# Kernel tuning notes

Hardware: AMD Instinct MI355X
Metric: run time of the kernel (lower is better)

The kernel has to match this reference:

```python
import jax, jax.numpy as jnp
import numpy as np

B, D, H, L = 65536, 512, 1024, 64
LOG2PI = float(np.log(2.0 * np.pi))


def setup_inputs() -> dict:
    key = jax.random.key(0)
    ks = jax.random.split(key, 16)
    s = jnp.float32(0.02)

    def w(k, shape):
        return jax.random.normal(k, shape, dtype=jnp.float32) * s

    return {
        "x": jax.random.normal(ks[0], (B, D), dtype=jnp.float32),
        "eps": jax.random.normal(ks[1], (B, L), dtype=jnp.float32),
        # encoder params (Linear stored as [in, out] for x @ W + b)
        "W_enc_h": w(ks[2], (D, H)), "b_enc_h": jnp.zeros((H,), jnp.float32),
        "W_enc_mu": w(ks[3], (H, L)), "b_enc_mu": jnp.zeros((L,), jnp.float32),
        "W_enc_lv": w(ks[4], (H, L)), "b_enc_lv": jnp.zeros((L,), jnp.float32),
        # decoder params
        "W_dec_h": w(ks[5], (L, H)), "b_dec_h": jnp.zeros((H,), jnp.float32),
        "W_dec_mu": w(ks[6], (H, D)), "b_dec_mu": jnp.zeros((D,), jnp.float32),
        "W_dec_lv": w(ks[7], (H, D)), "b_dec_lv": jnp.zeros((D,), jnp.float32),
    }


def reference(x, eps, W_enc_h, b_enc_h, W_enc_mu, b_enc_mu, W_enc_lv, b_enc_lv,
              W_dec_h, b_dec_h, W_dec_mu, b_dec_mu, W_dec_lv, b_dec_lv):
    beta = jnp.float32(1.0)
    # encoder
    h = jnp.tanh(x @ W_enc_h + b_enc_h)                      # [B, H]
    mu_z = h @ W_enc_mu + b_enc_mu                           # [B, L]
    lv_z = h @ W_enc_lv + b_enc_lv                           # [B, L]
    # reparameterised sample
    z = mu_z + jnp.exp(0.5 * lv_z) * eps                     # [B, L]
    # decoder
    hd = jnp.tanh(z @ W_dec_h + b_dec_h)                     # [B, H]
    mu_x = jax.nn.softmax(hd @ W_dec_mu + b_dec_mu, axis=-1) # [B, D]
    lv_x = hd @ W_dec_lv + b_dec_lv                          # [B, D]
    # KL(q(z|x) || N(0, I))
    kl = -0.5 * jnp.sum(1.0 + lv_z - mu_z ** 2 - jnp.exp(lv_z), axis=-1)  # [B]
    # diagonal Gaussian log-likelihood (closed form of MultivariateNormal
    # with diag_embed(exp(ln_var)) covariance)
    ln_pxz = -0.5 * jnp.sum(lv_x + (x - mu_x) ** 2 * jnp.exp(-lv_x) + LOG2PI, axis=-1)  # [B]
    return jnp.mean(ln_pxz - beta * kl)
```

## Files before the change

kernel.cpp:

```cpp
#include <hip/hip_runtime.h>

typedef unsigned char u8;
typedef unsigned short u16;
typedef unsigned int u32;
typedef long i64;
typedef __attribute__((ext_vector_type(2))) long long2v;
typedef __attribute__((ext_vector_type(4))) float floatx4;

#define LOG2PI_F 1.8378770664093453f

__device__ __forceinline__ u16 f2bf(float f) {
  union { float f; u32 i; } c; c.f = f;
  u32 i = c.i;
  u32 r = (i + 0x7fffu + ((i >> 16) & 1u)) >> 16;
  return (u16)r;
}
__device__ __forceinline__ float bf2f(u16 u) {
  union { u32 i; float f; } c; c.i = ((u32)u) << 16; return c.f;
}
__device__ __forceinline__ u8 f2fp8(float f) {
  int p = __builtin_amdgcn_cvt_pk_fp8_f32(f, f, 0, false);
  return (u8)(p & 0xff);
}
__device__ __forceinline__ u32 pk4fp8(float a, float b, float c, float d) {
  int lo = __builtin_amdgcn_cvt_pk_fp8_f32(a, b, 0, false);
  int v  = __builtin_amdgcn_cvt_pk_fp8_f32(c, d, lo, true);
  return (u32)v;
}
__device__ __forceinline__ void llds16(const void* g, void* l) {
  __builtin_amdgcn_global_load_lds(
      (const __attribute__((address_space(1))) u32*)g,
      (__attribute__((address_space(3))) u32*)l, 16, 0, 0);
}
__device__ __forceinline__ u32 permk(u32 k) {
  u32 g = k & ~63u, o = (k >> 3) & 7u, r = k & 7u;
  u32 po = ((o & 3u) << 1) | (o >> 2);
  return g | (po << 3) | r;
}

#define INV_4096  2.44140625e-4f
#define INV_16384 6.103515625e-5f

__global__ void pack_xb(const float* __restrict__ in, u32* __restrict__ out, int n4) {
  int i = blockIdx.x * 256 + threadIdx.x;
  if (i >= n4) return;
  const float4 v = ((const float4*)in)[i];
  int row = i >> 7;
  int k = (i & 127) << 2;
  int kp = permk(k);
  out[(row << 7) + (kp >> 2)] = pk4fp8(v.x * 16.f, v.y * 16.f, v.z * 16.f, v.w * 16.f);
}

__global__ void pack_wt(const float* __restrict__ W, u8* __restrict__ Wt, int K, int N) {
  int idx = blockIdx.x * 256 + threadIdx.x;
  if (idx >= K * N) return;
  int k = idx / N, n = idx - k * N;
  Wt[(size_t)n * K + permk(k)] = f2fp8(W[idx] * 256.f);
}

__global__ void pack_wt2(const float* __restrict__ W1, const float* __restrict__ W2,
                         u8* __restrict__ Wt, int K, int N1, int N2) {
  int idx = blockIdx.x * 256 + threadIdx.x;
  if (idx >= (N1 + N2) * K) return;
  int n = idx / K, k = idx - n * K;
  float v = (n < N1) ? W1[(size_t)k * N1 + n] : W2[(size_t)k * N2 + (n - N1)];
  Wt[(size_t)n * K + permk(k)] = f2fp8(v * 256.f);
}

__global__ void catf(const float* __restrict__ a, const float* __restrict__ b,
                     float* __restrict__ o, int n1, int n2) {
  int i = blockIdx.x * 256 + threadIdx.x;
  if (i < n1) o[i] = a[i];
  else if (i < n1 + n2) o[i] = b[i - n1];
}

template <int EPI>
__global__ __launch_bounds__(256) void gemm_bt(
    const u8* __restrict__ A, const u8* __restrict__ Bt,
    const float* __restrict__ bias, void* __restrict__ Cv,
    float inv, float outs, int M, int N, int K) {
  __shared__ __align__(16) u8 As[128 * 64];
  __shared__ __align__(16) u8 Bs[128 * 64];
  const int t = threadIdx.x;
  const int wave = t >> 6, lane = t & 63;
  const int quad = lane >> 4, l16 = lane & 15;
  const int bm = blockIdx.y * 128, bn = blockIdx.x * 128;
  const int wm = (wave >> 1) * 64, wn = (wave & 1) * 64;

  floatx4 acc[4][4];
#pragma unroll
  for (int i = 0; i < 4; ++i)
#pragma unroll
    for (int j = 0; j < 4; ++j) acc[i][j] = (floatx4){0.f, 0.f, 0.f, 0.f};

  for (int kt = 0; kt < K; kt += 64) {
#pragma unroll
    for (int i = 0; i < 2; ++i) {
      int c = i * 256 + t;
      int r = c >> 2, kcS = c & 3;
      int kc = kcS ^ ((r >> 1) & 3);
      llds16(A + (size_t)(bm + r) * K + kt + kc * 16, &As[c * 16]);
      llds16(Bt + (size_t)(bn + r) * K + kt + kc * 16, &Bs[c * 16]);
    }
    __builtin_amdgcn_s_waitcnt(0);
    __syncthreads();

    long2v a2[4], b2[4];
#pragma unroll
    for (int mi = 0; mi < 4; ++mi) {
      int m = wm + mi * 16 + l16;
      a2[mi] = *(const long2v*)&As[(4 * m + (quad ^ ((m >> 1) & 3))) * 16];
    }
#pragma unroll
    for (int ni = 0; ni < 4; ++ni) {
      int n = wn + ni * 16 + l16;
      b2[ni] = *(const long2v*)&Bs[(4 * n + (quad ^ ((n >> 1) & 3))) * 16];
    }
#pragma unroll
    for (int h = 0; h < 2; ++h)
#pragma unroll
      for (int mi = 0; mi < 4; ++mi)
#pragma unroll
        for (int ni = 0; ni < 4; ++ni)
          acc[mi][ni] = __builtin_amdgcn_mfma_f32_16x16x32_fp8_fp8(
              a2[mi][h], b2[ni][h], acc[mi][ni], 0, 0, 0);
    __syncthreads();
  }

#pragma unroll
  for (int ni = 0; ni < 4; ++ni) {
    int col = bn + wn + ni * 16 + l16;
    float bv = bias[col];
#pragma unroll
    for (int mi = 0; mi < 4; ++mi) {
#pragma unroll
      for (int r = 0; r < 4; ++r) {
        int row = bm + wm + mi * 16 + quad * 4 + r;
        float v = acc[mi][ni][r] * inv + bv;
        if (EPI == 0) {
          ((u8*)Cv)[(size_t)row * N + permk(col)] = f2fp8(tanhf(v) * outs);
        } else {
          ((u16*)Cv)[(size_t)row * N + col] = f2bf(v);
        }
      }
    }
  }
}

__global__ __launch_bounds__(256) void gemm_z(
    const u8* __restrict__ A, const u8* __restrict__ Bt,
    const float* __restrict__ bias, const float* __restrict__ eps,
    u8* __restrict__ z, float* __restrict__ accp, int M, int K) {
  __shared__ __align__(16) u8 As[128 * 64];
  __shared__ __align__(16) u8 Bs[128 * 64];
  __shared__ float sexp[128 * 64];
  const int t = threadIdx.x;
  const int wave = t >> 6, lane = t & 63;
  const int quad = lane >> 4, l16 = lane & 15;
  const int bm = blockIdx.y * 128;
  const int wm = (wave >> 1) * 64, wn = (wave & 1) * 64;

  floatx4 acc[4][4];
#pragma unroll
  for (int i = 0; i < 4; ++i)
#pragma unroll
    for (int j = 0; j < 4; ++j) acc[i][j] = (floatx4){0.f, 0.f, 0.f, 0.f};

  for (int kt = 0; kt < K; kt += 64) {
#pragma unroll
    for (int i = 0; i < 2; ++i) {
      int c = i * 256 + t;
      int r = c >> 2, kcS = c & 3;
      int kc = kcS ^ ((r >> 1) & 3);
      llds16(A + (size_t)(bm + r) * K + kt + kc * 16, &As[c * 16]);
      llds16(Bt + (size_t)r * K + kt + kc * 16, &Bs[c * 16]);
    }
    __builtin_amdgcn_s_waitcnt(0);
    __syncthreads();

    long2v a2[4], b2[4];
#pragma unroll
    for (int mi = 0; mi < 4; ++mi) {
      int m = wm + mi * 16 + l16;
      a2[mi] = *(const long2v*)&As[(4 * m + (quad ^ ((m >> 1) & 3))) * 16];
    }
#pragma unroll
    for (int ni = 0; ni < 4; ++ni) {
      int n = wn + ni * 16 + l16;
      b2[ni] = *(const long2v*)&Bs[(4 * n + (quad ^ ((n >> 1) & 3))) * 16];
    }
#pragma unroll
    for (int h = 0; h < 2; ++h)
#pragma unroll
      for (int mi = 0; mi < 4; ++mi)
#pragma unroll
        for (int ni = 0; ni < 4; ++ni)
          acc[mi][ni] = __builtin_amdgcn_mfma_f32_16x16x32_fp8_fp8(
              a2[mi][h], b2[ni][h], acc[mi][ni], 0, 0, 0);
    __syncthreads();
  }

  const bool is_lv = (wave & 1);
  float kl = 0.f;
#pragma unroll
  for (int ni = 0; ni < 4; ++ni) {
    int col = wn + ni * 16 + l16;
    float bv = bias[col];
#pragma unroll
    for (int mi = 0; mi < 4; ++mi) {
#pragma unroll
      for (int r = 0; r < 4; ++r) {
        int row = wm + mi * 16 + quad * 4 + r;
        float v = acc[mi][ni][r] * INV_16384 + bv;
        if (is_lv) {
          kl += 1.0f + v - __expf(v);
          sexp[row * 64 + (col - 64)] = __expf(0.5f * v);
        } else {
          kl -= v * v;
        }
      }
    }
  }
  __syncthreads();
  if (!is_lv) {
#pragma unroll
    for (int ni = 0; ni < 4; ++ni) {
      int col = wn + ni * 16 + l16;
      float bv = bias[col];
#pragma unroll
      for (int mi = 0; mi < 4; ++mi) {
#pragma unroll
        for (int r = 0; r < 4; ++r) {
          int row = wm + mi * 16 + quad * 4 + r;
          float mu = acc[mi][ni][r] * INV_16384 + bv;
          size_t grow = (size_t)(bm + row);
          float ep = eps[grow * 64 + col];
          z[grow * 64 + permk(col)] = f2fp8((mu + sexp[row * 64 + col] * ep) * 16.f);
        }
      }
    }
  }
  kl *= 0.5f;
  for (int off = 32; off > 0; off >>= 1) kl += __shfl_xor(kl, off, 64);
  __shared__ float s4[4];
  if (lane == 0) s4[wave] = kl;
  __syncthreads();
  if (t == 0) atomicAdd(accp, s4[0] + s4[1] + s4[2] + s4[3]);
}

__global__ __launch_bounds__(256) void lik_kernel(
    const u16* __restrict__ loglv, const float* __restrict__ x,
    float* __restrict__ acc) {
  typedef __attribute__((ext_vector_type(8))) short short8;
  const int wave = threadIdx.x >> 6, lane = threadIdx.x & 63;
  float wacc = 0.f;
  for (int rr = 0; rr < 8; ++rr) {
    int row = blockIdx.x * 32 + wave * 8 + rr;
    const u16* Lr = loglv + (size_t)row * 1024;
    short8 lg8 = ((const short8*)Lr)[lane];
    float lg[8];
#pragma unroll
    for (int j = 0; j < 8; ++j) lg[j] = bf2f((u16)lg8[j]);
    float mx = lg[0];
#pragma unroll
    for (int j = 1; j < 8; ++j) mx = fmaxf(mx, lg[j]);
    for (int off = 32; off > 0; off >>= 1) mx = fmaxf(mx, __shfl_xor(mx, off, 64));
    float e[8], s = 0.f;
#pragma unroll
    for (int j = 0; j < 8; ++j) { e[j] = __expf(lg[j] - mx); s += e[j]; }
    for (int off = 32; off > 0; off >>= 1) s += __shfl_xor(s, off, 64);
    float inv_s = 1.0f / s;
    short8 lv8 = ((const short8*)Lr)[64 + lane];
    const float* xr = x + (size_t)row * 512 + lane * 8;
    float4 x0 = *(const float4*)xr, x1 = *(const float4*)(xr + 4);
    float xs[8] = {x0.x, x0.y, x0.z, x0.w, x1.x, x1.y, x1.z, x1.w};
    float T = 0.f;
#pragma unroll
    for (int j = 0; j < 8; ++j) {
      float lv = bf2f((u16)lv8[j]);
      float d = xs[j] - e[j] * inv_s;
      T += lv + d * d * __expf(-lv) + LOG2PI_F;
    }
    for (int off = 32; off > 0; off >>= 1) T += __shfl_xor(T, off, 64);
    if (lane == 0) wacc += -0.5f * T;
  }
  __shared__ float s4[4];
  if (lane == 0) s4[wave] = wacc;
  __syncthreads();
  if (threadIdx.x == 0) atomicAdd(acc, s4[0] + s4[1] + s4[2] + s4[3]);
}

__global__ void fin_kernel(const float* __restrict__ acc, float* __restrict__ out) {
  out[0] = acc[0] * (1.0f / 65536.0f);
}

extern "C" void kernel_launch(void* const* d_in, const int* in_sizes, int n_in,
                              void* d_out, int out_size, void* d_ws, size_t ws_size,
                              hipStream_t stream) {
  const int B = 65536, D = 512, H = 1024, L = 64;
  const float* x       = (const float*)d_in[0];
  const float* eps     = (const float*)d_in[1];
  const float* W_enc_h = (const float*)d_in[2];
  const float* b_enc_h = (const float*)d_in[3];
  const float* W_enc_mu= (const float*)d_in[4];
  const float* b_enc_mu= (const float*)d_in[5];
  const float* W_enc_lv= (const float*)d_in[6];
  const float* b_enc_lv= (const float*)d_in[7];
  const float* W_dec_h = (const float*)d_in[8];
  const float* b_dec_h = (const float*)d_in[9];
  const float* W_dec_mu= (const float*)d_in[10];
  const float* b_dec_mu= (const float*)d_in[11];
  const float* W_dec_lv= (const float*)d_in[12];
  const float* b_dec_lv= (const float*)d_in[13];

  char* ws = (char*)d_ws;
  u8*   Wt_eh  = (u8*)(ws + 0);
  u8*   Wt_z   = (u8*)(ws + 524288);
  u8*   Wt_dh  = (u8*)(ws + 655360);
  u8*   Wt_dx  = (u8*)(ws + 720896);
  float* bh    = (float*)(ws + 2097152);
  float* bz    = (float*)(ws + 2101248);
  float* bdh   = (float*)(ws + 2105344);
  float* bdx   = (float*)(ws + 2109440);
  float* acc   = (float*)(ws + 2113536);
  u8*   hbuf   = (u8*)(ws + 4194304);
  u8*   xb     = (u8*)(ws + 71303168);
  u8*   zbuf   = (u8*)(ws + 104857600);
  u16*  loglv  = (u16*)(ws + 109051904);

  hipMemsetAsync(acc, 0, 256, stream);

  pack_xb<<<(B * D / 4 + 255) / 256, 256, 0, stream>>>(x, (u32*)xb, B * D / 4);
  pack_wt<<<(D * H + 255) / 256, 256, 0, stream>>>(W_enc_h, Wt_eh, D, H);
  pack_wt2<<<(H * 2 * L + 255) / 256, 256, 0, stream>>>(W_enc_mu, W_enc_lv, Wt_z, H, L, L);
  pack_wt<<<(L * H + 255) / 256, 256, 0, stream>>>(W_dec_h, Wt_dh, L, H);
  pack_wt2<<<(H * 2 * D + 255) / 256, 256, 0, stream>>>(W_dec_mu, W_dec_lv, Wt_dx, H, D, D);
  catf<<<(H + 255) / 256, 256, 0, stream>>>(b_enc_h, b_enc_h, bh, H, 0);
  catf<<<(2 * L + 255) / 256, 256, 0, stream>>>(b_enc_mu, b_enc_lv, bz, L, L);
  catf<<<(H + 255) / 256, 256, 0, stream>>>(b_dec_h, b_dec_h, bdh, H, 0);
  catf<<<(2 * D + 255) / 256, 256, 0, stream>>>(b_dec_mu, b_dec_lv, bdx, D, D);

  gemm_bt<0><<<dim3(H / 128, B / 128), 256, 0, stream>>>(
      xb, Wt_eh, bh, hbuf, INV_4096, 64.f, B, H, D);
  gemm_z<<<dim3(1, B / 128), 256, 0, stream>>>(hbuf, Wt_z, bz, eps, zbuf, acc, B, H);
  gemm_bt<0><<<dim3(H / 128, B / 128), 256, 0, stream>>>(
      zbuf, Wt_dh, bdh, hbuf, INV_4096, 64.f, B, H, L);
  gemm_bt<2><<<dim3(1024 / 128, B / 128), 256, 0, stream>>>(
      hbuf, Wt_dx, bdx, loglv, INV_16384, 0.f, B, 1024, H);
  lik_kernel<<<B / 32, 256, 0, stream>>>(loglv, x, acc);
  fin_kernel<<<1, 1, 0, stream>>>(acc, (float*)d_out);
}
```

Before: 619.0 us.

## Fuse decoder output GEMM with softmax and Gaussian likelihood reduction

```diff
diff --git a/kernel.cpp b/kernel.cpp
--- a/kernel.cpp
+++ b/kernel.cpp
@@ -9,15 +9,6 @@
 
 #define LOG2PI_F 1.8378770664093453f
 
-__device__ __forceinline__ u16 f2bf(float f) {
-  union { float f; u32 i; } c; c.f = f;
-  u32 i = c.i;
-  u32 r = (i + 0x7fffu + ((i >> 16) & 1u)) >> 16;
-  return (u16)r;
-}
-__device__ __forceinline__ float bf2f(u16 u) {
-  union { u32 i; float f; } c; c.i = ((u32)u) << 16; return c.f;
-}
 __device__ __forceinline__ u8 f2fp8(float f) {
   int p = __builtin_amdgcn_cvt_pk_fp8_f32(f, f, 0, false);
   return (u8)(p & 0xff);
@@ -26,6 +17,12 @@
   int lo = __builtin_amdgcn_cvt_pk_fp8_f32(a, b, 0, false);
   int v  = __builtin_amdgcn_cvt_pk_fp8_f32(c, d, lo, true);
   return (u32)v;
+}
+__device__ __forceinline__ void up4fp8(u32 pk, float* o) {
+  o[0] = __builtin_amdgcn_cvt_f32_fp8(pk, 0);
+  o[1] = __builtin_amdgcn_cvt_f32_fp8(pk, 1);
+  o[2] = __builtin_amdgcn_cvt_f32_fp8(pk, 2);
+  o[3] = __builtin_amdgcn_cvt_f32_fp8(pk, 3);
 }
 __device__ __forceinline__ void llds16(const void* g, void* l) {
   __builtin_amdgcn_global_load_lds(
@@ -67,17 +64,21 @@
   Wt[(size_t)n * K + permk(k)] = f2fp8(v * 256.f);
 }
 
-__global__ void catf(const float* __restrict__ a, const float* __restrict__ b,
-                     float* __restrict__ o, int n1, int n2) {
+__global__ void catb(const float* __restrict__ beh, const float* __restrict__ bem,
+                     const float* __restrict__ bel, const float* __restrict__ bdhi,
+                     const float* __restrict__ bdm, const float* __restrict__ bdl,
+                     float* __restrict__ bh, float* __restrict__ bz,
+                     float* __restrict__ bdh, float* __restrict__ bdx) {
   int i = blockIdx.x * 256 + threadIdx.x;
-  if (i < n1) o[i] = a[i];
-  else if (i < n1 + n2) o[i] = b[i - n1];
-}
-
-template <int EPI>
+  if (i < 1024) bh[i] = beh[i];
+  else if (i < 1152) { int j = i - 1024; bz[j] = (j < 64) ? bem[j] : bel[j - 64]; }
+  else if (i < 2176) { int j = i - 1152; bdh[j] = bdhi[j]; }
+  else if (i < 3200) { int j = i - 2176; bdx[j] = (j < 512) ? bdm[j] : bdl[j - 512]; }
+}
+
 __global__ __launch_bounds__(256) void gemm_bt(
     const u8* __restrict__ A, const u8* __restrict__ Bt,
-    const float* __restrict__ bias, void* __restrict__ Cv,
+    const float* __restrict__ bias, u8* __restrict__ Cv,
     float inv, float outs, int M, int N, int K) {
   __shared__ __align__(16) u8 As[128 * 64];
   __shared__ __align__(16) u8 Bs[128 * 64];
@@ -137,11 +138,7 @@
       for (int r = 0; r < 4; ++r) {
         int row = bm + wm + mi * 16 + quad * 4 + r;
         float v = acc[mi][ni][r] * inv + bv;
-        if (EPI == 0) {
-          ((u8*)Cv)[(size_t)row * N + permk(col)] = f2fp8(tanhf(v) * outs);
-        } else {
-          ((u16*)Cv)[(size_t)row * N + col] = f2bf(v);
-        }
+        Cv[(size_t)row * N + permk(col)] = f2fp8(tanhf(v) * outs);
       }
     }
   }
@@ -248,50 +245,143 @@
   if (t == 0) atomicAdd(accp, s4[0] + s4[1] + s4[2] + s4[3]);
 }
 
-__global__ __launch_bounds__(256) void lik_kernel(
-    const u16* __restrict__ loglv, const float* __restrict__ x,
-    float* __restrict__ acc) {
-  typedef __attribute__((ext_vector_type(8))) short short8;
-  const int wave = threadIdx.x >> 6, lane = threadIdx.x & 63;
-  float wacc = 0.f;
-  for (int rr = 0; rr < 8; ++rr) {
-    int row = blockIdx.x * 32 + wave * 8 + rr;
-    const u16* Lr = loglv + (size_t)row * 1024;
-    short8 lg8 = ((const short8*)Lr)[lane];
-    float lg[8];
-#pragma unroll
-    for (int j = 0; j < 8; ++j) lg[j] = bf2f((u16)lg8[j]);
-    float mx = lg[0];
-#pragma unroll
-    for (int j = 1; j < 8; ++j) mx = fmaxf(mx, lg[j]);
-    for (int off = 32; off > 0; off >>= 1) mx = fmaxf(mx, __shfl_xor(mx, off, 64));
-    float e[8], s = 0.f;
-#pragma unroll
-    for (int j = 0; j < 8; ++j) { e[j] = __expf(lg[j] - mx); s += e[j]; }
-    for (int off = 32; off > 0; off >>= 1) s += __shfl_xor(s, off, 64);
-    float inv_s = 1.0f / s;
-    short8 lv8 = ((const short8*)Lr)[64 + lane];
-    const float* xr = x + (size_t)row * 512 + lane * 8;
-    float4 x0 = *(const float4*)xr, x1 = *(const float4*)(xr + 4);
-    float xs[8] = {x0.x, x0.y, x0.z, x0.w, x1.x, x1.y, x1.z, x1.w};
-    float T = 0.f;
-#pragma unroll
-    for (int j = 0; j < 8; ++j) {
-      float lv = bf2f((u16)lv8[j]);
-      float d = xs[j] - e[j] * inv_s;
-      T += lv + d * d * __expf(-lv) + LOG2PI_F;
-    }
-    for (int off = 32; off > 0; off >>= 1) T += __shfl_xor(T, off, 64);
-    if (lane == 0) wacc += -0.5f * T;
-  }
+#define PPAD 136
+__global__ __launch_bounds__(256) void gemm_lik(
+    const u8* __restrict__ A, const u8* __restrict__ Bt,
+    const float* __restrict__ bias, const float* __restrict__ x,
+    float* __restrict__ accp, int M, int K) {
+  __shared__ __align__(16) u8 As[128 * 64];
+  __shared__ __align__(16) u8 Plds[512 * PPAD];
+  __shared__ float srow[128 * 2];
   __shared__ float s4[4];
-  if (lane == 0) s4[wave] = wacc;
+  const int t = threadIdx.x;
+  const int wave = t >> 6, lane = t & 63;
+  const int quad = lane >> 4, l16 = lane & 15;
+  const int bm = blockIdx.x * 128;
+  const int wm = (wave >> 1) * 64, wn = (wave & 1) * 64;
+
+  float rsum[16];
+#pragma unroll
+  for (int i = 0; i < 16; ++i) rsum[i] = 0.f;
+  float invs[16];
+  float wT = 0.f;
+
+  for (int nt = 0; nt < 8; ++nt) {
+    floatx4 acc[4][4];
+#pragma unroll
+    for (int i = 0; i < 4; ++i)
+#pragma unroll
+      for (int j = 0; j < 4; ++j) acc[i][j] = (floatx4){0.f, 0.f, 0.f, 0.f};
+
+    for (int kt = 0; kt < K; kt += 64) {
+#pragma unroll
+      for (int i = 0; i < 2; ++i) {
+        int c = i * 256 + t;
+        int r = c >> 2, kcS = c & 3;
+        int kc = kcS ^ ((r >> 1) & 3);
+        llds16(A + (size_t)(bm + r) * K + kt + kc * 16, &As[c * 16]);
+      }
+      long2v b2[4];
+#pragma unroll
+      for (int ni = 0; ni < 4; ++ni) {
+        int n = nt * 128 + wn + ni * 16 + l16;
+        b2[ni] = *(const long2v*)(Bt + (size_t)n * K + kt + quad * 16);
+      }
+      __builtin_amdgcn_s_waitcnt(0);
+      __syncthreads();
+
+      long2v a2[4];
+#pragma unroll
+      for (int mi = 0; mi < 4; ++mi) {
+        int m = wm + mi * 16 + l16;
+        a2[mi] = *(const long2v*)&As[(4 * m + (quad ^ ((m >> 1) & 3))) * 16];
+      }
+#pragma unroll
+      for (int h = 0; h < 2; ++h)
+#pragma unroll
+        for (int mi = 0; mi < 4; ++mi)
+#pragma unroll
+          for (int ni = 0; ni < 4; ++ni)
+            acc[mi][ni] = __builtin_amdgcn_mfma_f32_16x16x32_fp8_fp8(
+                a2[mi][h], b2[ni][h], acc[mi][ni], 0, 0, 0);
+      __syncthreads();
+    }
+
+    if (nt < 4) {
+#pragma unroll
+      for (int ni = 0; ni < 4; ++ni) {
+        int col = nt * 128 + wn + ni * 16 + l16;
+        float bv = bias[col];
+#pragma unroll
+        for (int mi = 0; mi < 4; ++mi) {
+          int rowb = wm + mi * 16 + quad * 4;
+          float ev[4];
+#pragma unroll
+          for (int r = 0; r < 4; ++r) {
+            float v = acc[mi][ni][r] * INV_16384 + bv;
+            ev[r] = __expf(v);
+            rsum[mi * 4 + r] += ev[r];
+          }
+          *(u32*)&Plds[(size_t)col * PPAD + rowb] = pk4fp8(ev[0], ev[1], ev[2], ev[3]);
+        }
+      }
+      if (nt == 3) {
+#pragma unroll
+        for (int i = 0; i < 16; ++i) {
+          rsum[i] += __shfl_xor(rsum[i], 1, 64);
+          rsum[i] += __shfl_xor(rsum[i], 2, 64);
+          rsum[i] += __shfl_xor(rsum[i], 4, 64);
+          rsum[i] += __shfl_xor(rsum[i], 8, 64);
+        }
+        if (l16 == 0) {
+#pragma unroll
+          for (int mi = 0; mi < 4; ++mi)
+#pragma unroll
+            for (int r = 0; r < 4; ++r)
+              srow[(wm + mi * 16 + quad * 4 + r) * 2 + (wave & 1)] = rsum[mi * 4 + r];
+        }
+        __syncthreads();
+#pragma unroll
+        for (int mi = 0; mi < 4; ++mi)
+#pragma unroll
+          for (int r = 0; r < 4; ++r) {
+            int row = wm + mi * 16 + quad * 4 + r;
+            invs[mi * 4 + r] = 1.0f / (srow[row * 2] + srow[row * 2 + 1]);
+          }
+      }
+    } else {
+#pragma unroll
+      for (int ni = 0; ni < 4; ++ni) {
+        int col = nt * 128 + wn + ni * 16 + l16;
+        int colx = col - 512;
+        float bv = bias[col];
+#pragma unroll
+        for (int mi = 0; mi < 4; ++mi) {
+          int rowb = wm + mi * 16 + quad * 4;
+          u32 pk = *(const u32*)&Plds[(size_t)colx * PPAD + rowb];
+          float pv[4];
+          up4fp8(pk, pv);
+#pragma unroll
+          for (int r = 0; r < 4; ++r) {
+            float lv = acc[mi][ni][r] * INV_16384 + bv;
+            float p = pv[r] * invs[mi * 4 + r];
+            float xv = x[(size_t)(bm + rowb + r) * 512 + colx];
+            float d = xv - p;
+            wT += lv + d * d * __expf(-lv);
+          }
+        }
+      }
+    }
+  }
+
+  for (int off = 32; off > 0; off >>= 1) wT += __shfl_xor(wT, off, 64);
+  if (lane == 0) s4[wave] = wT;
   __syncthreads();
-  if (threadIdx.x == 0) atomicAdd(acc, s4[0] + s4[1] + s4[2] + s4[3]);
+  if (t == 0) atomicAdd(accp, -0.5f * (s4[0] + s4[1] + s4[2] + s4[3]));
 }
 
 __global__ void fin_kernel(const float* __restrict__ acc, float* __restrict__ out) {
-  out[0] = acc[0] * (1.0f / 65536.0f);
+  out[0] = acc[0] * (1.0f / 65536.0f) - 256.0f * LOG2PI_F;
 }
 
 extern "C" void kernel_launch(void* const* d_in, const int* in_sizes, int n_in,
@@ -326,27 +416,22 @@
   u8*   hbuf   = (u8*)(ws + 4194304);
   u8*   xb     = (u8*)(ws + 71303168);
   u8*   zbuf   = (u8*)(ws + 104857600);
-  u16*  loglv  = (u16*)(ws + 109051904);
-
-  hipMemsetAsync(acc, 0, 256, stream);
+
+  (void)hipMemsetAsync(acc, 0, 256, stream);
 
   pack_xb<<<(B * D / 4 + 255) / 256, 256, 0, stream>>>(x, (u32*)xb, B * D / 4);
   pack_wt<<<(D * H + 255) / 256, 256, 0, stream>>>(W_enc_h, Wt_eh, D, H);
   pack_wt2<<<(H * 2 * L + 255) / 256, 256, 0, stream>>>(W_enc_mu, W_enc_lv, Wt_z, H, L, L);
   pack_wt<<<(L * H + 255) / 256, 256, 0, stream>>>(W_dec_h, Wt_dh, L, H);
   pack_wt2<<<(H * 2 * D + 255) / 256, 256, 0, stream>>>(W_dec_mu, W_dec_lv, Wt_dx, H, D, D);
-  catf<<<(H + 255) / 256, 256, 0, stream>>>(b_enc_h, b_enc_h, bh, H, 0);
-  catf<<<(2 * L + 255) / 256, 256, 0, stream>>>(b_enc_mu, b_enc_lv, bz, L, L);
-  catf<<<(H + 255) / 256, 256, 0, stream>>>(b_dec_h, b_dec_h, bdh, H, 0);
-  catf<<<(2 * D + 255) / 256, 256, 0, stream>>>(b_dec_mu, b_dec_lv, bdx, D, D);
-
-  gemm_bt<0><<<dim3(H / 128, B / 128), 256, 0, stream>>>(
+  catb<<<13, 256, 0, stream>>>(b_enc_h, b_enc_mu, b_enc_lv, b_dec_h, b_dec_mu, b_dec_lv,
+                               bh, bz, bdh, bdx);
+
+  gemm_bt<<<dim3(H / 128, B / 128), 256, 0, stream>>>(
       xb, Wt_eh, bh, hbuf, INV_4096, 64.f, B, H, D);
   gemm_z<<<dim3(1, B / 128), 256, 0, stream>>>(hbuf, Wt_z, bz, eps, zbuf, acc, B, H);
-  gemm_bt<0><<<dim3(H / 128, B / 128), 256, 0, stream>>>(
+  gemm_bt<<<dim3(H / 128, B / 128), 256, 0, stream>>>(
       zbuf, Wt_dh, bdh, hbuf, INV_4096, 64.f, B, H, L);
-  gemm_bt<2><<<dim3(1024 / 128, B / 128), 256, 0, stream>>>(
-      hbuf, Wt_dx, bdx, loglv, INV_16384, 0.f, B, 1024, H);
-  lik_kernel<<<B / 32, 256, 0, stream>>>(loglv, x, acc);
+  gemm_lik<<<B / 128, 256, 0, stream>>>(hbuf, Wt_dx, bdx, x, acc, B, H);
   fin_kernel<<<1, 1, 0, stream>>>(acc, (float*)d_out);
 }
```

Measured after the change: 743.8 us. 1.2x slower.
